# Kernel optimization log

Measured on AMD Instinct MI355X. Metric: run time of the kernel, lower is better.

## Reference

```python
import jax, jax.numpy as jnp
import numpy as np
from jax import lax

N = 120000    # active voxels at coarse (input) level
NUP = 240000  # active voxels after transposed upsample (matches skip)
CIN = 128
COUT = 64
BN_EPS = 1e-5


def _sparse_conv(feats, W, idx_in, idx_out, n_out):
    """Gather->matmul->scatter-add sparse conv.
    feats: [N_in, Cin]; W: [K, Cin, Cout]; idx_in/idx_out: [K, M] int32.
    Loops over the K kernel offsets via lax.scan (K is small and fixed)."""
    out0 = jnp.zeros((n_out, W.shape[-1]), feats.dtype)

    def body(acc, kmap):
        Wk, ik, ok = kmap
        contrib = jnp.take(feats, ik, axis=0) @ Wk  # [M, Cout]
        return acc.at[ok].add(contrib), None

    out, _ = lax.scan(body, out0, (W, idx_in, idx_out))
    return out


def _bn(x, g, b):
    # BatchNorm1d in training mode: per-channel stats over all voxels (biased var)
    m = jnp.mean(x, axis=0)
    v = jnp.mean(jnp.square(x - m), axis=0)
    return (x - m) * lax.rsqrt(v + BN_EPS) * g + b


def setup_inputs() -> dict:
    key = jax.random.key(0)
    ks = jax.random.split(key, 20)
    f32 = jnp.float32
    inp = {
        "x_F": jax.random.normal(ks[0], (N, CIN), f32),
        "skip_F": jax.random.normal(ks[1], (NUP, COUT), f32),
        "W_trans": jax.random.normal(ks[2], (27, CIN, COUT), f32) * 0.02,
        "W_up": jax.random.normal(ks[3], (27, COUT, COUT), f32) * 0.02,
        "W1": jax.random.normal(ks[4], (9, COUT, COUT), f32) * 0.02,
        "W2": jax.random.normal(ks[5], (9, COUT, COUT), f32) * 0.02,
        "W3": jax.random.normal(ks[6], (27, COUT, COUT), f32) * 0.02,
        "g0": jnp.ones((COUT,), f32), "b0": jnp.zeros((COUT,), f32),
        "g1": jnp.ones((COUT,), f32), "b1": jnp.zeros((COUT,), f32),
        "g2": jnp.ones((COUT,), f32), "b2": jnp.zeros((COUT,), f32),
        "g3": jnp.ones((COUT,), f32), "b3": jnp.zeros((COUT,), f32),
        "mt_in": jax.random.randint(ks[7], (27, N), 0, N, jnp.int32),
        "mt_out": jax.random.randint(ks[8], (27, N), 0, N, jnp.int32),
        "mu_in": jax.random.randint(ks[9], (27, NUP), 0, N, jnp.int32),
        "mu_out": jax.random.randint(ks[10], (27, NUP), 0, NUP, jnp.int32),
        "m1_in": jax.random.randint(ks[11], (9, NUP), 0, NUP, jnp.int32),
        "m1_out": jax.random.randint(ks[12], (9, NUP), 0, NUP, jnp.int32),
        "m2_in": jax.random.randint(ks[13], (9, NUP), 0, NUP, jnp.int32),
        "m2_out": jax.random.randint(ks[14], (9, NUP), 0, NUP, jnp.int32),
        "m3_in": jax.random.randint(ks[15], (27, NUP), 0, NUP, jnp.int32),
        "m3_out": jax.random.randint(ks[16], (27, NUP), 0, NUP, jnp.int32),
    }
    return inp


def reference(x_F, skip_F, W_trans, W_up, W1, W2, W3,
              g0, b0, g1, b1, g2, b2, g3, b3,
              mt_in, mt_out, mu_in, mu_out,
              m1_in, m1_out, m2_in, m2_out, m3_in, m3_out):
    lrelu = jax.nn.leaky_relu  # default negative_slope=0.01 matches nn.LeakyReLU
    # trans_dilao (3x3x3 submanifold) -> LeakyReLU -> BN
    upA = _bn(lrelu(_sparse_conv(x_F, W_trans, mt_in, mt_out, N)), g0, b0)
    # transposed upsample conv to NUP voxels, then residual add with skip
    upA = _sparse_conv(upA, W_up, mu_in, mu_out, NUP) + skip_F
    # conv1 (1x3x3) -> act -> bn
    upE = _bn(lrelu(_sparse_conv(upA, W1, m1_in, m1_out, NUP)), g1, b1)
    # conv2 (3x1x3) -> act -> bn
    upE = _bn(lrelu(_sparse_conv(upE, W2, m2_in, m2_out, NUP)), g2, b2)
    # conv3 (3x3x3) -> act -> bn
    upE = _bn(lrelu(_sparse_conv(upE, W3, m3_in, m3_out, NUP)), g3, b3)
    return upE
```

## Files before the change

kernel.cpp:

```cpp
#include <hip/hip_runtime.h>

#define N_VOX   120000
#define NUP_VOX 240000
constexpr float BN_EPS = 1e-5f;

__device__ __forceinline__ float lrelu(float x) { return x >= 0.f ? x : 0.01f * x; }

template <int CIN, int ROWS>
__global__ __launch_bounds__(256) void sconv_kernel(
    const float* __restrict__ feats, const float* __restrict__ W,
    const int* __restrict__ idx_in, const int* __restrict__ idx_out,
    float* __restrict__ out, int M)
{
    const int lane = threadIdx.x & 63;
    const int wv   = threadIdx.x >> 6;
    const int k    = blockIdx.y;

    float wreg[CIN];
    const float* Wk = W + (size_t)k * CIN * 64;
#pragma unroll
    for (int ci = 0; ci < CIN; ++ci) wreg[ci] = Wk[ci * 64 + lane];

    const int* ikp = idx_in  + (size_t)k * M;
    const int* okp = idx_out + (size_t)k * M;

    const int stride = gridDim.x * 4 * ROWS;
    for (int m0 = (blockIdx.x * 4 + wv) * ROWS; m0 < M; m0 += stride) {
#pragma unroll
        for (int r = 0; r < ROWS; ++r) {
            int m = m0 + r;
            if (ROWS > 1 && m >= M) break;
            int ik = __builtin_amdgcn_readfirstlane(ikp[m]);
            int ok = __builtin_amdgcn_readfirstlane(okp[m]);
            const float* __restrict__ row = feats + (size_t)ik * CIN;
            float a0 = 0.f, a1 = 0.f, a2 = 0.f, a3 = 0.f;
#pragma unroll
            for (int ci = 0; ci < CIN; ci += 4) {
                a0 = fmaf(row[ci + 0], wreg[ci + 0], a0);
                a1 = fmaf(row[ci + 1], wreg[ci + 1], a1);
                a2 = fmaf(row[ci + 2], wreg[ci + 2], a2);
                a3 = fmaf(row[ci + 3], wreg[ci + 3], a3);
            }
            atomicAdd(out + (size_t)ok * 64 + lane, (a0 + a1) + (a2 + a3));
        }
    }
}

__global__ __launch_bounds__(256) void stats_kernel(
    const float* __restrict__ x, int R, float* __restrict__ st)
{
    const int lane = threadIdx.x & 63;
    const int wv   = threadIdx.x >> 6;
    float s = 0.f, q = 0.f;
    const int stride = gridDim.x * 4;
    for (int r = blockIdx.x * 4 + wv; r < R; r += stride) {
        float v = lrelu(x[(size_t)r * 64 + lane]);
        s += v;
        q = fmaf(v, v, q);
    }
    __shared__ float ls[4][64];
    __shared__ float lq[4][64];
    ls[wv][lane] = s;
    lq[wv][lane] = q;
    __syncthreads();
    if (wv == 0) {
        float S = ls[0][lane] + ls[1][lane] + ls[2][lane] + ls[3][lane];
        float Q = lq[0][lane] + lq[1][lane] + lq[2][lane] + lq[3][lane];
        atomicAdd(&st[lane], S);
        atomicAdd(&st[64 + lane], Q);
    }
}

__global__ __launch_bounds__(256) void bn_apply_kernel(
    const float* __restrict__ x, float* __restrict__ y,
    const float* __restrict__ st, const float* __restrict__ g,
    const float* __restrict__ b, int R)
{
    __shared__ float sc[64];
    __shared__ float sh[64];
    const float invR = 1.f / (float)R;
    if (threadIdx.x < 64) {
        int ch = threadIdx.x;
        float m = st[ch] * invR;
        float v = st[64 + ch] * invR - m * m;
        float s = rsqrtf(v + BN_EPS) * g[ch];
        sc[ch] = s;
        sh[ch] = fmaf(-m, s, b[ch]);
    }
    __syncthreads();

    const size_t total = (size_t)R * 16;
    size_t i = (size_t)blockIdx.x * blockDim.x + threadIdx.x;
    const size_t stride = (size_t)gridDim.x * blockDim.x;
    const float4* xv = (const float4*)x;
    float4* yv = (float4*)y;
    for (; i < total; i += stride) {
        int ch = (int)((i * 4) & 63);
        float4 v = xv[i];
        float4 o;
        o.x = fmaf(lrelu(v.x), sc[ch + 0], sh[ch + 0]);
        o.y = fmaf(lrelu(v.y), sc[ch + 1], sh[ch + 1]);
        o.z = fmaf(lrelu(v.z), sc[ch + 2], sh[ch + 2]);
        o.w = fmaf(lrelu(v.w), sc[ch + 3], sh[ch + 3]);
        yv[i] = o;
    }
}

extern "C" void kernel_launch(void* const* d_in, const int* in_sizes, int n_in,
                              void* d_out, int out_size, void* d_ws, size_t ws_size,
                              hipStream_t stream)
{
    const float* x_F   = (const float*)d_in[0];
    const float* skipF = (const float*)d_in[1];
    const float* Wt    = (const float*)d_in[2];
    const float* Wu    = (const float*)d_in[3];
    const float* W1    = (const float*)d_in[4];
    const float* W2    = (const float*)d_in[5];
    const float* W3    = (const float*)d_in[6];
    const float* g0 = (const float*)d_in[7];
    const float* b0 = (const float*)d_in[8];
    const float* g1 = (const float*)d_in[9];
    const float* b1 = (const float*)d_in[10];
    const float* g2 = (const float*)d_in[11];
    const float* b2 = (const float*)d_in[12];
    const float* g3 = (const float*)d_in[13];
    const float* b3 = (const float*)d_in[14];
    const int* mt_in  = (const int*)d_in[15];
    const int* mt_out = (const int*)d_in[16];
    const int* mu_in  = (const int*)d_in[17];
    const int* mu_out = (const int*)d_in[18];
    const int* m1_in  = (const int*)d_in[19];
    const int* m1_out = (const int*)d_in[20];
    const int* m2_in  = (const int*)d_in[21];
    const int* m2_out = (const int*)d_in[22];
    const int* m3_in  = (const int*)d_in[23];
    const int* m3_out = (const int*)d_in[24];

    float* s0 = (float*)d_ws;
    float* s1 = s0 + (size_t)N_VOX * 64;
    float* st = s1 + (size_t)NUP_VOX * 64;
    float* s2 = (float*)d_out;

    const dim3 blk(256);
    const int CB = 512;

    hipMemsetAsync(s0, 0, (size_t)N_VOX * 64 * sizeof(float), stream);
    hipMemsetAsync(st, 0, 128 * sizeof(float), stream);
    sconv_kernel<128, 1><<<dim3(CB, 27), blk, 0, stream>>>(x_F, Wt, mt_in, mt_out, s0, N_VOX);
    stats_kernel<<<dim3(768), blk, 0, stream>>>(s0, N_VOX, st);
    bn_apply_kernel<<<dim3(1024), blk, 0, stream>>>(s0, s0, st, g0, b0, N_VOX);

    hipMemcpyAsync(s1, skipF, (size_t)NUP_VOX * 64 * sizeof(float),
                   hipMemcpyDeviceToDevice, stream);
    sconv_kernel<64, 2><<<dim3(CB, 27), blk, 0, stream>>>(s0, Wu, mu_in, mu_out, s1, NUP_VOX);

    hipMemsetAsync(s2, 0, (size_t)NUP_VOX * 64 * sizeof(float), stream);
    hipMemsetAsync(st, 0, 128 * sizeof(float), stream);
    sconv_kernel<64, 2><<<dim3(CB, 9), blk, 0, stream>>>(s1, W1, m1_in, m1_out, s2, NUP_VOX);
    stats_kernel<<<dim3(768), blk, 0, stream>>>(s2, NUP_VOX, st);
    bn_apply_kernel<<<dim3(2048), blk, 0, stream>>>(s2, s2, st, g1, b1, NUP_VOX);

    hipMemsetAsync(s1, 0, (size_t)NUP_VOX * 64 * sizeof(float), stream);
    hipMemsetAsync(st, 0, 128 * sizeof(float), stream);
    sconv_kernel<64, 2><<<dim3(CB, 9), blk, 0, stream>>>(s2, W2, m2_in, m2_out, s1, NUP_VOX);
    stats_kernel<<<dim3(768), blk, 0, stream>>>(s1, NUP_VOX, st);
    bn_apply_kernel<<<dim3(2048), blk, 0, stream>>>(s1, s1, st, g2, b2, NUP_VOX);

    hipMemsetAsync(s2, 0, (size_t)NUP_VOX * 64 * sizeof(float), stream);
    hipMemsetAsync(st, 0, 128 * sizeof(float), stream);
    sconv_kernel<64, 2><<<dim3(CB, 27), blk, 0, stream>>>(s1, W3, m3_in, m3_out, s2, NUP_VOX);
    stats_kernel<<<dim3(768), blk, 0, stream>>>(s2, NUP_VOX, st);
    bn_apply_kernel<<<dim3(2048), blk, 0, stream>>>(s2, s2, st, g3, b3, NUP_VOX);
}
```

Measured before the change: 5.890 ms.

## Replace per-row wave sparse conv with LDS-tiled gather-GEMM-scatter kernel

The sparse conv kernel now gathers a tile of TE input rows into LDS (transposed), keeps the full weight slice in LDS, and computes a register-blocked TMx4 outer-product tile per thread before scattering the results with atomics. The goal is to replace one wave per row doing scalar broadcast loads with a small GEMM that reuses each gathered row across 64 output channels and each weight across many rows. In exchange, atomic writes are split into four per-thread scalar atomics with a different coalescing pattern. The code also assumes M is a multiple of TE and adds two barriers per tile.

```diff
diff --git a/kernel.cpp b/kernel.cpp
--- a/kernel.cpp
+++ b/kernel.cpp
@@ -6,42 +6,88 @@
 
 __device__ __forceinline__ float lrelu(float x) { return x >= 0.f ? x : 0.01f * x; }
 
-template <int CIN, int ROWS>
-__global__ __launch_bounds__(256) void sconv_kernel(
+template <int CIN, int TE>
+__global__ __launch_bounds__(256) void sconv_gemm_kernel(
     const float* __restrict__ feats, const float* __restrict__ W,
     const int* __restrict__ idx_in, const int* __restrict__ idx_out,
     float* __restrict__ out, int M)
 {
-    const int lane = threadIdx.x & 63;
-    const int wv   = threadIdx.x >> 6;
-    const int k    = blockIdx.y;
-
-    float wreg[CIN];
-    const float* Wk = W + (size_t)k * CIN * 64;
-#pragma unroll
-    for (int ci = 0; ci < CIN; ++ci) wreg[ci] = Wk[ci * 64 + lane];
+    constexpr int PAD = TE + 4;
+    constexpr int TM  = TE / 16;
+    constexpr int TPE = 256 / TE;
+    constexpr int CPT = CIN / TPE;
+
+    __shared__ float At[CIN][PAD];
+    __shared__ float Wl[CIN][64];
+    __shared__ int   okl[TE];
+
+    const int t  = threadIdx.x;
+    const int k  = blockIdx.y;
+    const int tn = t & 15;
+    const int tm = t >> 4;
+    const int e  = t / TPE;
+    const int sc = t % TPE;
+
+    const float4* Wk4 = (const float4*)(W + (size_t)k * CIN * 64);
+    for (int i = t; i < CIN * 16; i += 256)
+        ((float4*)&Wl[0][0])[i] = Wk4[i];
 
     const int* ikp = idx_in  + (size_t)k * M;
     const int* okp = idx_out + (size_t)k * M;
 
-    const int stride = gridDim.x * 4 * ROWS;
-    for (int m0 = (blockIdx.x * 4 + wv) * ROWS; m0 < M; m0 += stride) {
-#pragma unroll
-        for (int r = 0; r < ROWS; ++r) {
-            int m = m0 + r;
-            if (ROWS > 1 && m >= M) break;
-            int ik = __builtin_amdgcn_readfirstlane(ikp[m]);
-            int ok = __builtin_amdgcn_readfirstlane(okp[m]);
-            const float* __restrict__ row = feats + (size_t)ik * CIN;
-            float a0 = 0.f, a1 = 0.f, a2 = 0.f, a3 = 0.f;
-#pragma unroll
-            for (int ci = 0; ci < CIN; ci += 4) {
-                a0 = fmaf(row[ci + 0], wreg[ci + 0], a0);
-                a1 = fmaf(row[ci + 1], wreg[ci + 1], a1);
-                a2 = fmaf(row[ci + 2], wreg[ci + 2], a2);
-                a3 = fmaf(row[ci + 3], wreg[ci + 3], a3);
+    for (int tile = blockIdx.x; tile * TE < M; tile += gridDim.x) {
+        const int m0 = tile * TE;
+        __syncthreads();
+        if (t < TE) okl[t] = okp[m0 + t];
+        const int ik = ikp[m0 + e];
+        const float4* row4 = (const float4*)(feats + (size_t)ik * CIN + sc * CPT);
+        float4 v[CPT / 4];
+#pragma unroll
+        for (int j = 0; j < CPT / 4; ++j) v[j] = row4[j];
+#pragma unroll
+        for (int j = 0; j < CPT / 4; ++j) {
+            const int ci = sc * CPT + j * 4;
+            At[ci + 0][e] = v[j].x;
+            At[ci + 1][e] = v[j].y;
+            At[ci + 2][e] = v[j].z;
+            At[ci + 3][e] = v[j].w;
+        }
+        __syncthreads();
+
+        float acc[TM][4];
+#pragma unroll
+        for (int i = 0; i < TM; ++i)
+#pragma unroll
+            for (int j = 0; j < 4; ++j) acc[i][j] = 0.f;
+
+#pragma unroll 4
+        for (int ci = 0; ci < CIN; ++ci) {
+            float a[TM];
+            if constexpr (TM == 4) {
+                float4 av = *(const float4*)&At[ci][tm * 4];
+                a[0] = av.x; a[1] = av.y; a[2] = av.z; a[3] = av.w;
+            } else {
+                float2 av = *(const float2*)&At[ci][tm * 2];
+                a[0] = av.x; a[1] = av.y;
             }
-            atomicAdd(out + (size_t)ok * 64 + lane, (a0 + a1) + (a2 + a3));
+            float4 b = *(const float4*)&Wl[ci][tn * 4];
+#pragma unroll
+            for (int i = 0; i < TM; ++i) {
+                acc[i][0] = fmaf(a[i], b.x, acc[i][0]);
+                acc[i][1] = fmaf(a[i], b.y, acc[i][1]);
+                acc[i][2] = fmaf(a[i], b.z, acc[i][2]);
+                acc[i][3] = fmaf(a[i], b.w, acc[i][3]);
+            }
+        }
+
+#pragma unroll
+        for (int i = 0; i < TM; ++i) {
+            const int o = okl[tm * TM + i];
+            float* po = out + (size_t)o * 64 + tn * 4;
+            atomicAdd(po + 0, acc[i][0]);
+            atomicAdd(po + 1, acc[i][1]);
+            atomicAdd(po + 2, acc[i][2]);
+            atomicAdd(po + 3, acc[i][3]);
         }
     }
 }
@@ -142,33 +188,32 @@
     float* s2 = (float*)d_out;
 
     const dim3 blk(256);
-    const int CB = 512;
 
     hipMemsetAsync(s0, 0, (size_t)N_VOX * 64 * sizeof(float), stream);
     hipMemsetAsync(st, 0, 128 * sizeof(float), stream);
-    sconv_kernel<128, 1><<<dim3(CB, 27), blk, 0, stream>>>(x_F, Wt, mt_in, mt_out, s0, N_VOX);
+    sconv_gemm_kernel<128, 32><<<dim3(64, 27), blk, 0, stream>>>(x_F, Wt, mt_in, mt_out, s0, N_VOX);
     stats_kernel<<<dim3(768), blk, 0, stream>>>(s0, N_VOX, st);
     bn_apply_kernel<<<dim3(1024), blk, 0, stream>>>(s0, s0, st, g0, b0, N_VOX);
 
     hipMemcpyAsync(s1, skipF, (size_t)NUP_VOX * 64 * sizeof(float),
                    hipMemcpyDeviceToDevice, stream);
-    sconv_kernel<64, 2><<<dim3(CB, 27), blk, 0, stream>>>(s0, Wu, mu_in, mu_out, s1, NUP_VOX);
+    sconv_gemm_kernel<64, 64><<<dim3(64, 27), blk, 0, stream>>>(s0, Wu, mu_in, mu_out, s1, NUP_VOX);
 
     hipMemsetAsync(s2, 0, (size_t)NUP_VOX * 64 * sizeof(float), stream);
     hipMemsetAsync(st, 0, 128 * sizeof(float), stream);
-    sconv_kernel<64, 2><<<dim3(CB, 9), blk, 0, stream>>>(s1, W1, m1_in, m1_out, s2, NUP_VOX);
+    sconv_gemm_kernel<64, 64><<<dim3(192, 9), blk, 0, stream>>>(s1, W1, m1_in, m1_out, s2, NUP_VOX);
     stats_kernel<<<dim3(768), blk, 0, stream>>>(s2, NUP_VOX, st);
     bn_apply_kernel<<<dim3(2048), blk, 0, stream>>>(s2, s2, st, g1, b1, NUP_VOX);
 
     hipMemsetAsync(s1, 0, (size_t)NUP_VOX * 64 * sizeof(float), stream);
     hipMemsetAsync(st, 0, 128 * sizeof(float), stream);
-    sconv_kernel<64, 2><<<dim3(CB, 9), blk, 0, stream>>>(s2, W2, m2_in, m2_out, s1, NUP_VOX);
+    sconv_gemm_kernel<64, 64><<<dim3(192, 9), blk, 0, stream>>>(s2, W2, m2_in, m2_out, s1, NUP_VOX);
     stats_kernel<<<dim3(768), blk, 0, stream>>>(s1, NUP_VOX, st);
     bn_apply_kernel<<<dim3(2048), blk, 0, stream>>>(s1, s1, st, g2, b2, NUP_VOX);
 
     hipMemsetAsync(s2, 0, (size_t)NUP_VOX * 64 * sizeof(float), stream);
     hipMemsetAsync(st, 0, 128 * sizeof(float), stream);
-    sconv_kernel<64, 2><<<dim3(CB, 27), blk, 0, stream>>>(s1, W3, m3_in, m3_out, s2, NUP_VOX);
+    sconv_gemm_kernel<64, 64><<<dim3(64, 27), blk, 0, stream>>>(s1, W3, m3_in, m3_out, s2, NUP_VOX);
     stats_kernel<<<dim3(768), blk, 0, stream>>>(s2, NUP_VOX, st);
     bn_apply_kernel<<<dim3(2048), blk, 0, stream>>>(s2, s2, st, g3, b3, NUP_VOX);
 }
```

Result: slower. 18.09 ms (+207.1%).
